# Kernel optimization log

Measured on AMD Instinct MI355X. Metric: run time of the kernel, lower is better.

The kernel has to match this reference:

```python
import jax, jax.numpy as jnp
import numpy as np

THRESHOLD = 0.5
NEG_RATIO = 3
ALPHA = 1.0
IMG_SIZE = 300.0  # convert_to_ratio divides pixel coords by image size


def _ssd300_default_boxes():
    """Canonical SSD300 priors: 8732 boxes in (cx, cy, w, h), clipped to [0,1]."""
    fmaps = [38, 19, 10, 5, 3, 1]
    scales = [0.1, 0.2, 0.375, 0.55, 0.725, 0.9]
    ars = [[1.0, 2.0, 0.5],
           [1.0, 2.0, 3.0, 0.5, 1.0 / 3.0],
           [1.0, 2.0, 3.0, 0.5, 1.0 / 3.0],
           [1.0, 2.0, 3.0, 0.5, 1.0 / 3.0],
           [1.0, 2.0, 0.5],
           [1.0, 2.0, 0.5]]
    boxes = []
    for k, (f, s) in enumerate(zip(fmaps, scales)):
        for i in range(f):
            for j in range(f):
                cx = (j + 0.5) / f
                cy = (i + 0.5) / f
                for ar in ars[k]:
                    boxes.append([cx, cy, s * np.sqrt(ar), s / np.sqrt(ar)])
                    if ar == 1.0:
                        s2 = np.sqrt(s * scales[k + 1]) if k < len(fmaps) - 1 else 1.0
                        boxes.append([cx, cy, s2, s2])
    return np.clip(np.asarray(boxes, dtype=np.float32), 0.0, 1.0)  # (8732, 4)


def _cxcy_to_xy(b):
    return jnp.concatenate([b[..., :2] - b[..., 2:] / 2.0,
                            b[..., :2] + b[..., 2:] / 2.0], axis=-1)


def _iou(a, b):
    # a: [N,4] xyxy, b: [P,4] xyxy -> [N,P]
    lt = jnp.maximum(a[:, None, :2], b[None, :, :2])
    rb = jnp.minimum(a[:, None, 2:], b[None, :, 2:])
    wh = jnp.clip(rb - lt, 0.0)
    inter = wh[..., 0] * wh[..., 1]
    area_a = (a[:, 2] - a[:, 0]) * (a[:, 3] - a[:, 1])
    area_b = (b[:, 2] - b[:, 0]) * (b[:, 3] - b[:, 1])
    return inter / (area_a[:, None] + area_b[None, :] - inter)


def _encode_cxcy(t, d):
    # standard SSD offsets (variances 0.1, 0.2). Safe log for unmatched (zero) boxes
    # -- those entries are masked out of the loss, matching torch's positive-only gather.
    g_cxcy = (t[..., :2] - d[..., :2]) / (d[..., 2:] / 10.0)
    safe_wh = jnp.where(t[..., 2:] > 0.0, t[..., 2:], d[..., 2:])
    g_wh = jnp.log(safe_wh / d[..., 2:]) * 5.0
    return jnp.concatenate([g_cxcy, g_wh], axis=-1)


def setup_inputs() -> dict:
    key = jax.random.key(0)
    k1, k2, k3, k4 = jax.random.split(key, 4)
    B, P, C, N = 128, 8732, 81, 16
    predicted_boxes = jax.random.normal(k1, (B, P, 4), dtype=jnp.float32)
    predicted_scores = jax.random.normal(k2, (B, P, C), dtype=jnp.float32)
    u = jax.random.uniform(k3, (B, N, 4), dtype=jnp.float32)
    cxcy = (0.15 + 0.7 * u[..., :2]) * IMG_SIZE   # centers in pixel coords
    wh = (0.08 + 0.32 * u[..., 2:]) * IMG_SIZE    # sizes in pixel coords
    target_boxes = jnp.concatenate([cxcy, wh], axis=-1)
    target_labels = jax.random.randint(k4, (B, N), 1, C)
    default_boxes = jnp.asarray(_ssd300_default_boxes())
    return {"predicted_boxes": predicted_boxes,
            "predicted_scores": predicted_scores,
            "target_boxes": target_boxes,
            "target_labels": target_labels,
            "default_boxes": default_boxes}


def reference(predicted_boxes, predicted_scores, target_boxes, target_labels, default_boxes):
    B, P, C = predicted_scores.shape
    db_xy = _cxcy_to_xy(default_boxes)
    tb = target_boxes / IMG_SIZE  # convert_to_ratio

    def match(boxes, labels):
        # boxes: [N,4] cxcywh (ratio), labels: [N]
        ov = _iou(_cxcy_to_xy(boxes), db_xy)          # [N, P]
        best_ov = ov.max(axis=0)                      # [P]
        obj_idx = ov.argmax(axis=0)                   # [P]
        box_idx = ov.argmax(axis=1)                   # [N] best prior per object
        obj_idx = obj_idx.at[box_idx].set(jnp.arange(boxes.shape[0]))
        check = best_ov > THRESHOLD                   # uses pre-scatter max (faithful)
        t_lab = jnp.where(check, labels[obj_idx], 0)
        t_box = jnp.where(check[:, None], boxes[obj_idx], 0.0)
        return _encode_cxcy(t_box, default_boxes), t_lab

    true_bboxes, true_labels = jax.vmap(match)(tb, target_labels)  # [B,P,4], [B,P]

    positive = true_labels != 0                        # [B,P]
    n_pos = jnp.maximum(positive.sum(), 1)

    # SmoothL1 (beta=1), mean over positive elements (num_pos * 4)
    diff = jnp.abs(predicted_boxes - true_bboxes)
    sl1 = jnp.where(diff < 1.0, 0.5 * diff * diff, diff - 0.5)
    bbox_loss = (sl1 * positive[..., None]).sum() / (n_pos.astype(sl1.dtype) * 4.0)

    # per-box cross entropy
    logp = jax.nn.log_softmax(predicted_scores, axis=-1)
    cls_all = -jnp.take_along_axis(logp, true_labels[..., None], axis=-1)[..., 0]  # [B,P]

    cls_pos_sum = (cls_all * positive).sum()
    neg = jnp.where(positive, 0.0, cls_all)
    neg_sorted = -jnp.sort(-neg, axis=1)               # descending per image
    n_hard = positive.sum(axis=1) * NEG_RATIO          # [B]
    rank = jnp.arange(P)[None, :]
    hard_neg_sum = (neg_sorted * (rank < n_hard[:, None])).sum()

    cls_loss = (cls_pos_sum + hard_neg_sum) / n_pos.astype(cls_all.dtype)
    return cls_loss + ALPHA * bbox_loss
```

## Files before the change

### kernel.cpp

```cpp
#include <hip/hip_runtime.h>
#include <hip/hip_bf16.h>
#include <math.h>

#define BB 128
#define PP 8732
#define NN 16
#define CC 81
#define IMG 300.0f
#define K2_BLOCKS 4096
#define K1_THREADS 512

__global__ __launch_bounds__(K1_THREADS) void k1_match(
    const float* __restrict__ pred_boxes,
    const float* __restrict__ tgt_boxes,
    const int*   __restrict__ tgt_labels,
    const float* __restrict__ dboxes,
    int*   __restrict__ tlab_out,
    float* __restrict__ bbox_partial,
    int*   __restrict__ pos_count)
{
    const int b   = blockIdx.x;
    const int tid = threadIdx.x;
    const int NW  = K1_THREADS / 64;

    __shared__ float t_cx[NN], t_cy[NN], t_w[NN], t_h[NN];
    __shared__ float t_x0s[NN], t_y0s[NN], t_x1s[NN], t_y1s[NN], t_areas[NN];
    __shared__ int   t_lab[NN];
    __shared__ unsigned short obj_s[PP];
    __shared__ unsigned char  chk_s[PP];
    __shared__ float red_v[NN][NW];
    __shared__ int   red_i[NN][NW];
    __shared__ int   box_idx_s[NN];
    __shared__ float red_f[NW];
    __shared__ int   red_c[NW];

    if (tid < NN) {
        const float* tb = tgt_boxes + ((size_t)b * NN + tid) * 4;
        float cx = tb[0] / IMG, cy = tb[1] / IMG, w = tb[2] / IMG, h = tb[3] / IMG;
        t_cx[tid] = cx; t_cy[tid] = cy; t_w[tid] = w; t_h[tid] = h;
        float x0 = cx - w * 0.5f, y0 = cy - h * 0.5f;
        float x1 = cx + w * 0.5f, y1 = cy + h * 0.5f;
        t_x0s[tid] = x0; t_y0s[tid] = y0; t_x1s[tid] = x1; t_y1s[tid] = y1;
        t_areas[tid] = (x1 - x0) * (y1 - y0);
        t_lab[tid] = tgt_labels[(size_t)b * NN + tid];
    }
    __syncthreads();

    float tx0[NN], ty0[NN], tx1[NN], ty1[NN], tar[NN];
#pragma unroll
    for (int n = 0; n < NN; ++n) {
        tx0[n] = t_x0s[n]; ty0[n] = t_y0s[n];
        tx1[n] = t_x1s[n]; ty1[n] = t_y1s[n];
        tar[n] = t_areas[n];
    }

    float bestv[NN];
    int   bestp[NN];
#pragma unroll
    for (int n = 0; n < NN; ++n) { bestv[n] = -1e30f; bestp[n] = 0x7fffffff; }

    for (int p = tid; p < PP; p += K1_THREADS) {
        float4 d = *reinterpret_cast<const float4*>(dboxes + (size_t)p * 4);
        float dx0 = d.x - d.z * 0.5f, dy0 = d.y - d.w * 0.5f;
        float dx1 = d.x + d.z * 0.5f, dy1 = d.y + d.w * 0.5f;
        float dar = (dx1 - dx0) * (dy1 - dy0);
        float bov = -1.0f; int bidx = 0;
#pragma unroll
        for (int n = 0; n < NN; ++n) {
            float lx = fmaxf(tx0[n], dx0);
            float ly = fmaxf(ty0[n], dy0);
            float rx = fminf(tx1[n], dx1);
            float ry = fminf(ty1[n], dy1);
            float iw = fmaxf(rx - lx, 0.0f);
            float ih = fmaxf(ry - ly, 0.0f);
            float inter = iw * ih;
            float iou = inter / (tar[n] + dar - inter);
            if (iou > bov) { bov = iou; bidx = n; }
            if (iou > bestv[n]) { bestv[n] = iou; bestp[n] = p; }
        }
        obj_s[p] = (unsigned short)bidx;
        chk_s[p] = (bov > 0.5f) ? 1 : 0;
    }

#pragma unroll
    for (int n = 0; n < NN; ++n) {
        float v = bestv[n]; int ip = bestp[n];
        for (int off = 32; off; off >>= 1) {
            float v2 = __shfl_xor(v, off);
            int   p2 = __shfl_xor(ip, off);
            if (v2 > v || (v2 == v && p2 < ip)) { v = v2; ip = p2; }
        }
        if ((tid & 63) == 0) { red_v[n][tid >> 6] = v; red_i[n][tid >> 6] = ip; }
    }
    __syncthreads();
    if (tid < NN) {
        float v = red_v[tid][0]; int ip = red_i[tid][0];
        for (int w = 1; w < NW; ++w) {
            float v2 = red_v[tid][w]; int p2 = red_i[tid][w];
            if (v2 > v || (v2 == v && p2 < ip)) { v = v2; ip = p2; }
        }
        box_idx_s[tid] = ip;
    }
    __syncthreads();
    if (tid == 0) {
        for (int n = 0; n < NN; ++n) obj_s[box_idx_s[n]] = (unsigned short)n;
    }
    __syncthreads();

    float bacc = 0.0f;
    int   pcnt = 0;
    for (int p = tid; p < PP; p += K1_THREADS) {
        int lab = 0;
        if (chk_s[p]) {
            int n = obj_s[p];
            lab = t_lab[n];
            if (lab != 0) {
                ++pcnt;
                float4 d = *reinterpret_cast<const float4*>(dboxes + (size_t)p * 4);
                float gx = (t_cx[n] - d.x) / (d.z / 10.0f);
                float gy = (t_cy[n] - d.y) / (d.w / 10.0f);
                float gw = logf(t_w[n] / d.z) * 5.0f;
                float gh = logf(t_h[n] / d.w) * 5.0f;
                float4 pv = *reinterpret_cast<const float4*>(pred_boxes + ((size_t)b * PP + p) * 4);
                float dfs[4] = { pv.x - gx, pv.y - gy, pv.z - gw, pv.w - gh };
#pragma unroll
                for (int j = 0; j < 4; ++j) {
                    float ad = fabsf(dfs[j]);
                    bacc += (ad < 1.0f) ? 0.5f * ad * ad : ad - 0.5f;
                }
            }
        }
        tlab_out[(size_t)b * PP + p] = lab;
    }
    for (int off = 32; off; off >>= 1) {
        bacc += __shfl_xor(bacc, off);
        pcnt += __shfl_xor(pcnt, off);
    }
    if ((tid & 63) == 0) { red_f[tid >> 6] = bacc; red_c[tid >> 6] = pcnt; }
    __syncthreads();
    if (tid == 0) {
        float s = 0.0f; int c = 0;
        for (int w = 0; w < NW; ++w) { s += red_f[w]; c += red_c[w]; }
        bbox_partial[b] = s;
        pos_count[b]    = c;
    }
}

__global__ __launch_bounds__(256) void k2_cls(
    const float* __restrict__ scores,
    const int*   __restrict__ tlab,
    float* __restrict__ neg,
    float* __restrict__ clspos_partial)
{
    const long long ROWS = (long long)BB * PP;
    const int tid    = threadIdx.x;
    const int lane16 = tid & 15;
    const int grp    = tid >> 4;

    float acc = 0.0f;
    for (long long r0 = (long long)blockIdx.x * 16; r0 < ROWS;
         r0 += (long long)gridDim.x * 16) {
        long long r = r0 + grp;
        if (r < ROWS) {
            const float* row = scores + (size_t)r * CC;
            float x[6];
#pragma unroll
            for (int e = 0; e < 6; ++e) {
                int c = lane16 + e * 16;
                x[e] = (c < CC) ? row[c] : -1e30f;
            }
            float m = x[0];
#pragma unroll
            for (int e = 1; e < 6; ++e) m = fmaxf(m, x[e]);
            float s = 0.0f;
#pragma unroll
            for (int e = 0; e < 6; ++e) s += __expf(x[e] - m);
            for (int off = 8; off; off >>= 1) {
                float m2 = __shfl_xor(m, off);
                float s2 = __shfl_xor(s, off);
                float mn = fmaxf(m, m2);
                s = s * __expf(m - mn) + s2 * __expf(m2 - mn);
                m = mn;
            }
            if (lane16 == 0) {
                int   lab = tlab[r];
                float sl  = row[lab];
                float cls = m + __logf(s) - sl;
                if (lab != 0) { acc += cls; neg[r] = 0.0f; }
                else          { neg[r] = cls; }
            }
        }
    }
    for (int off = 32; off; off >>= 1) acc += __shfl_xor(acc, off);
    __shared__ float wsum[4];
    if ((tid & 63) == 0) wsum[tid >> 6] = acc;
    __syncthreads();
    if (tid == 0)
        clspos_partial[blockIdx.x] = wsum[0] + wsum[1] + wsum[2] + wsum[3];
}

__global__ __launch_bounds__(256) void k3_topk(
    const float* __restrict__ neg,
    const int*   __restrict__ pos_count,
    float* __restrict__ hard_partial)
{
    const int b   = blockIdx.x;
    const int tid = threadIdx.x;

    __shared__ unsigned int vals[PP];
    __shared__ int hist[256];
    __shared__ int scan[256];
    __shared__ unsigned int s_prefix;
    __shared__ int s_kk;
    __shared__ float wsum[4];

    for (int i = tid; i < PP; i += 256)
        vals[i] = __float_as_uint(neg[(size_t)b * PP + i]);

    int k = pos_count[b] * 3;
    if (k > PP) k = PP;
    if (k <= 0) {
        if (tid == 0) hard_partial[b] = 0.0f;
        return;
    }
    if (tid == 0) { s_prefix = 0u; s_kk = k; }
    __syncthreads();

    unsigned int prefmask = 0u;
    for (int round = 0; round < 4; ++round) {
        const int shift = 24 - 8 * round;
        hist[tid] = 0;
        __syncthreads();
        unsigned int pref = s_prefix;
        for (int i = tid; i < PP; i += 256) {
            unsigned int v = vals[i];
            if ((v & prefmask) == pref)
                atomicAdd(&hist[(v >> shift) & 0xFF], 1);
        }
        __syncthreads();
        scan[tid] = hist[tid];
        __syncthreads();
        for (int off = 1; off < 256; off <<= 1) {
            int add = (tid + off < 256) ? scan[tid + off] : 0;
            __syncthreads();
            scan[tid] += add;
            __syncthreads();
        }
        int sg = scan[tid] - hist[tid];
        int kk = s_kk;
        __syncthreads();
        if (sg < kk && sg + hist[tid] >= kk) {
            s_prefix = pref | ((unsigned int)tid << shift);
            s_kk     = kk - sg;
        }
        __syncthreads();
        prefmask |= (0xFFu << shift);
    }

    unsigned int t = s_prefix;
    int kk = s_kk;
    float tf = __uint_as_float(t);

    float acc = 0.0f;
    for (int i = tid; i < PP; i += 256) {
        unsigned int v = vals[i];
        if (v > t) acc += __uint_as_float(v);
    }
    for (int off = 32; off; off >>= 1) acc += __shfl_xor(acc, off);
    if ((tid & 63) == 0) wsum[tid >> 6] = acc;
    __syncthreads();
    if (tid == 0)
        hard_partial[b] = wsum[0] + wsum[1] + wsum[2] + wsum[3] + (float)kk * tf;
}

__global__ __launch_bounds__(256) void k4_final(
    const float* __restrict__ clspos_partial,
    const float* __restrict__ bbox_partial,
    const float* __restrict__ hard_partial,
    const int*   __restrict__ pos_count,
    float* __restrict__ out)
{
    const int tid = threadIdx.x;
    float cacc = 0.0f, bacc = 0.0f, hacc = 0.0f;
    int   pacc = 0;
    for (int i = tid; i < K2_BLOCKS; i += 256) cacc += clspos_partial[i];
    if (tid < BB) {
        bacc = bbox_partial[tid];
        hacc = hard_partial[tid];
        pacc = pos_count[tid];
    }
    __shared__ float sc[256], sb[256], sh[256];
    __shared__ int   sp[256];
    sc[tid] = cacc; sb[tid] = bacc; sh[tid] = hacc; sp[tid] = pacc;
    __syncthreads();
    for (int off = 128; off; off >>= 1) {
        if (tid < off) {
            sc[tid] += sc[tid + off];
            sb[tid] += sb[tid + off];
            sh[tid] += sh[tid + off];
            sp[tid] += sp[tid + off];
        }
        __syncthreads();
    }
    if (tid == 0) {
        float npos = fmaxf((float)sp[0], 1.0f);
        out[0] = (sc[0] + sh[0]) / npos + sb[0] / (npos * 4.0f);
    }
}

extern "C" void kernel_launch(void* const* d_in, const int* in_sizes, int n_in,
                              void* d_out, int out_size, void* d_ws, size_t ws_size,
                              hipStream_t stream) {
    const float* pred_boxes  = (const float*)d_in[0];
    const float* pred_scores = (const float*)d_in[1];
    const float* tgt_boxes   = (const float*)d_in[2];
    const int*   tgt_labels  = (const int*)d_in[3];
    const float* dboxes      = (const float*)d_in[4];
    float* out = (float*)d_out;

    char* ws = (char*)d_ws;
    int*   tlab           = (int*)ws;   ws += (size_t)BB * PP * sizeof(int);
    float* neg            = (float*)ws; ws += (size_t)BB * PP * sizeof(float);
    int*   pos_count      = (int*)ws;   ws += BB * sizeof(int);
    float* bbox_partial   = (float*)ws; ws += BB * sizeof(float);
    float* hard_partial   = (float*)ws; ws += BB * sizeof(float);
    float* clspos_partial = (float*)ws; ws += K2_BLOCKS * sizeof(float);

    k1_match<<<BB, K1_THREADS, 0, stream>>>(pred_boxes, tgt_boxes, tgt_labels, dboxes,
                                            tlab, bbox_partial, pos_count);
    k2_cls<<<K2_BLOCKS, 256, 0, stream>>>(pred_scores, tlab, neg, clspos_partial);
    k3_topk<<<BB, 256, 0, stream>>>(neg, pos_count, hard_partial);
    k4_final<<<1, 256, 0, stream>>>(clspos_partial, bbox_partial, hard_partial,
                                    pos_count, out);
}
```

Measured before the change: 171.0 us.

## Stage score tiles in LDS and compute one row per thread in k2

The per-row log-softmax kernel now copies contiguous tiles of 64 rows × 81 classes into shared memory with coalesced loads, then has each thread compute max/sum-exp over its own row serially. This replaces the old 16-lanes-per-row layout with shuffle reductions and strided per-row loads. Blocks shrink to one 64-thread wavefront with about 20 KB of LDS each. The risks are LDS bank conflicts, since the row stride of 81 is odd, which limits conflicts, and lower occupancy from the small blocks.

After: 213.7 us. 1.25x slower.

```diff
diff --git a/kernel.cpp b/kernel.cpp
--- a/kernel.cpp
+++ b/kernel.cpp
@@ -8,6 +8,9 @@
 #define CC 81
 #define IMG 300.0f
 #define K2_BLOCKS 4096
+#define K2_THREADS 64
+#define TILE_ROWS 64
+#define NT ((BB * PP) / TILE_ROWS)
 #define K1_THREADS 512
 
 __global__ __launch_bounds__(K1_THREADS) void k1_match(
@@ -146,57 +149,40 @@
     }
 }
 
-__global__ __launch_bounds__(256) void k2_cls(
+__global__ __launch_bounds__(K2_THREADS) void k2_cls(
     const float* __restrict__ scores,
     const int*   __restrict__ tlab,
     float* __restrict__ neg,
     float* __restrict__ clspos_partial)
 {
-    const long long ROWS = (long long)BB * PP;
-    const int tid    = threadIdx.x;
-    const int lane16 = tid & 15;
-    const int grp    = tid >> 4;
-
+    __shared__ float slds[TILE_ROWS * CC];
+    const int lane = threadIdx.x;
     float acc = 0.0f;
-    for (long long r0 = (long long)blockIdx.x * 16; r0 < ROWS;
-         r0 += (long long)gridDim.x * 16) {
-        long long r = r0 + grp;
-        if (r < ROWS) {
-            const float* row = scores + (size_t)r * CC;
-            float x[6];
-#pragma unroll
-            for (int e = 0; e < 6; ++e) {
-                int c = lane16 + e * 16;
-                x[e] = (c < CC) ? row[c] : -1e30f;
-            }
-            float m = x[0];
-#pragma unroll
-            for (int e = 1; e < 6; ++e) m = fmaxf(m, x[e]);
-            float s = 0.0f;
-#pragma unroll
-            for (int e = 0; e < 6; ++e) s += __expf(x[e] - m);
-            for (int off = 8; off; off >>= 1) {
-                float m2 = __shfl_xor(m, off);
-                float s2 = __shfl_xor(s, off);
-                float mn = fmaxf(m, m2);
-                s = s * __expf(m - mn) + s2 * __expf(m2 - mn);
-                m = mn;
-            }
-            if (lane16 == 0) {
-                int   lab = tlab[r];
-                float sl  = row[lab];
-                float cls = m + __logf(s) - sl;
-                if (lab != 0) { acc += cls; neg[r] = 0.0f; }
-                else          { neg[r] = cls; }
-            }
-        }
-    }
+
+    for (int t = blockIdx.x; t < NT; t += gridDim.x) {
+        const float* g = scores + (size_t)t * (TILE_ROWS * CC);
+        __syncthreads();
+        for (int i = lane; i < TILE_ROWS * CC; i += K2_THREADS)
+            slds[i] = g[i];
+        __syncthreads();
+
+        const float* myrow = &slds[lane * CC];
+        float m = myrow[0];
+#pragma unroll 16
+        for (int c = 1; c < CC; ++c) m = fmaxf(m, myrow[c]);
+        float s = 0.0f;
+#pragma unroll 16
+        for (int c = 0; c < CC; ++c) s += __expf(myrow[c] - m);
+
+        long long r = (long long)t * TILE_ROWS + lane;
+        int   lab = tlab[r];
+        float cls = m + __logf(s) - myrow[lab];
+        if (lab != 0) { acc += cls; neg[r] = 0.0f; }
+        else          { neg[r] = cls; }
+    }
+
     for (int off = 32; off; off >>= 1) acc += __shfl_xor(acc, off);
-    __shared__ float wsum[4];
-    if ((tid & 63) == 0) wsum[tid >> 6] = acc;
-    __syncthreads();
-    if (tid == 0)
-        clspos_partial[blockIdx.x] = wsum[0] + wsum[1] + wsum[2] + wsum[3];
+    if (lane == 0) clspos_partial[blockIdx.x] = acc;
 }
 
 __global__ __launch_bounds__(256) void k3_topk(
@@ -328,7 +314,7 @@
 
     k1_match<<<BB, K1_THREADS, 0, stream>>>(pred_boxes, tgt_boxes, tgt_labels, dboxes,
                                             tlab, bbox_partial, pos_count);
-    k2_cls<<<K2_BLOCKS, 256, 0, stream>>>(pred_scores, tlab, neg, clspos_partial);
+    k2_cls<<<K2_BLOCKS, K2_THREADS, 0, stream>>>(pred_scores, tlab, neg, clspos_partial);
     k3_topk<<<BB, 256, 0, stream>>>(neg, pos_count, hard_partial);
     k4_final<<<1, 256, 0, stream>>>(clspos_partial, bbox_partial, hard_partial,
                                     pos_count, out);
```
